# Kernel tuning notes

Measured on AMD Instinct MI355X. Metric: run time of the kernel, lower is better.

The kernel has to match this reference:

```python
import jax, jax.numpy as jnp
import numpy as np
import math

B, N, E, H = 2, 10000, 160000, 128
ET = 8
EPS = 1e-5


def setup_inputs() -> dict:
    key = jax.random.key(0)
    ks = jax.random.split(key, 20)
    s = 1.0 / math.sqrt(H)
    inp = {
        "hidden": jax.random.normal(ks[0], (B, N, H), jnp.float32),
        "time_emb": jax.random.normal(ks[1], (B, N, H), jnp.float32),
        "edge_index": jax.random.randint(ks[2], (2, E), 0, N),
        "edge_type": jax.random.randint(ks[3], (E,), 0, ET),
        # parameters
        "edge_emb": jax.random.normal(ks[4], (ET, H), jnp.float32),
        "Wq": jax.random.normal(ks[5], (H, H), jnp.float32) * s,
        "bq": jnp.zeros((H,), jnp.float32),
        "Wk": jax.random.normal(ks[6], (H, H), jnp.float32) * s,
        "bk": jnp.zeros((H,), jnp.float32),
        "Wv": jax.random.normal(ks[7], (H, H), jnp.float32) * s,
        "bv": jnp.zeros((H,), jnp.float32),
        "We": jax.random.normal(ks[8], (H, 1), jnp.float32) * s,
        "be": jnp.zeros((1,), jnp.float32),
        "W1": jax.random.normal(ks[9], (3 * H, H), jnp.float32) * (1.0 / math.sqrt(3 * H)),
        "b1": jnp.zeros((H,), jnp.float32),
        "W2": jax.random.normal(ks[10], (H, H), jnp.float32) * s,
        "b2": jnp.zeros((H,), jnp.float32),
        "gamma": jnp.ones((H,), jnp.float32),
        "beta": jnp.zeros((H,), jnp.float32),
    }
    return inp


def _forward(hidden, time_emb, edge_index, edge_type, edge_emb,
             Wq, bq, Wk, bk, Wv, bv, We, be, W1, b1, W2, b2, gamma, beta):
    src, tgt = edge_index[0], edge_index[1]
    # edge-wise gathers: [B, E, H]
    src_h = hidden[:, src]
    tgt_h = hidden[:, tgt]
    src_t = time_emb[:, src]
    tgt_t = time_emb[:, tgt]
    edge_h = edge_emb[edge_type][None, :, :]  # [1, E, H] broadcasts over batch

    query = (tgt_h + tgt_t) @ Wq + bq
    key = (src_h + src_t + edge_h) @ Wk + bk
    value = (src_h + edge_h) @ Wv + bv

    logits = jnp.einsum("beh,beh->be", query, key) / math.sqrt(H)
    logits = logits + (edge_h @ We + be)[..., 0]  # edge bias broadcast over batch

    # segment softmax per target node (equivalent to the per-node masked softmax loop)
    lT = logits.T  # [E, B]
    seg_max = jax.ops.segment_max(lT, tgt, num_segments=N)          # [N, B]
    seg_max = jnp.where(jnp.isfinite(seg_max), seg_max, 0.0)
    ex = jnp.exp(lT - seg_max[tgt])                                  # [E, B]
    seg_sum = jax.ops.segment_sum(ex, tgt, num_segments=N)           # [N, B]
    weights = (ex / seg_sum[tgt]).T                                  # [B, E]

    messages = value * weights[..., None]                            # [B, E, H]
    # scatter-add to target nodes
    agg = jax.ops.segment_sum(jnp.swapaxes(messages, 0, 1), tgt, num_segments=N)  # [N, B, H]
    aggregated = jnp.swapaxes(agg, 0, 1)                             # [B, N, H]

    cat = jnp.concatenate([hidden, aggregated, time_emb], axis=-1)   # [B, N, 3H]
    updated = jax.nn.silu(cat @ W1 + b1) @ W2 + b2

    x = hidden + updated  # dropout p=0 -> identity
    mu = jnp.mean(x, axis=-1, keepdims=True)
    var = jnp.var(x, axis=-1, keepdims=True)
    return (x - mu) * jax.lax.rsqrt(var + EPS) * gamma + beta


def reference(hidden, time_emb, edge_index, edge_type, edge_emb,
              Wq, bq, Wk, bk, Wv, bv, We, be, W1, b1, W2, b2, gamma, beta):
    return _forward(hidden, time_emb, edge_index, edge_type, edge_emb,
                    Wq, bq, Wk, bk, Wv, bv, We, be, W1, b1, W2, b2, gamma, beta)
```

## Files before the change

### kernel.cpp

```cpp
#include <hip/hip_runtime.h>
#include <math.h>

constexpr int B_  = 2;
constexpr int N_  = 10000;
constexpr int E_  = 160000;
constexpr int H_  = 128;
constexpr int ET_ = 8;
constexpr float EPS_ = 1e-5f;
constexpr float RSQH = 0.08838834764831845f;

typedef __bf16 bf16x8 __attribute__((ext_vector_type(8)));
typedef short  short8 __attribute__((ext_vector_type(8)));
typedef float  f32x4  __attribute__((ext_vector_type(4)));
typedef unsigned short u16;

__device__ inline u16 bf16b(float f) {
    return __builtin_bit_cast(u16, (__bf16)f);
}

__device__ inline bf16x8 ldfrag(const u16* __restrict__ W, int kc, int nt, int lane) {
    short8 s = *(const short8*)(W + ((kc * 8 + nt) * 64 + lane) * 8);
    return __builtin_bit_cast(bf16x8, s);
}

__global__ __launch_bounds__(256)
void setup_kernel(const float* __restrict__ W1, const float* __restrict__ W2,
                  const float* __restrict__ Wq, const float* __restrict__ Wk,
                  const float* __restrict__ Wv,
                  u16* __restrict__ W1s, u16* __restrict__ W2s,
                  u16* __restrict__ Wqs, u16* __restrict__ Wks, u16* __restrict__ Wvs,
                  const float* __restrict__ edge_emb,
                  const float* __restrict__ bk, const float* __restrict__ bv,
                  const float* __restrict__ We, const float* __restrict__ be,
                  float* __restrict__ Kt, float* __restrict__ Vt, float* __restrict__ eb,
                  const int* __restrict__ tgt, int* __restrict__ hist)
{
    const int bid = blockIdx.x, tid = threadIdx.x;
    if (bid < 56) {
        int unit = bid >> 1, half = bid & 1;
        const float* src; u16* dst; int kc;
        if (unit < 12)      { src = W1; dst = W1s; kc = unit; }
        else if (unit < 16) { src = W2; dst = W2s; kc = unit - 12; }
        else if (unit < 20) { src = Wq; dst = Wqs; kc = unit - 16; }
        else if (unit < 24) { src = Wk; dst = Wks; kc = unit - 20; }
        else                { src = Wv; dst = Wvs; kc = unit - 24; }
        int nt = half * 4 + (tid >> 6), lane = tid & 63;
        int q = lane >> 4, c = lane & 15;
        int kbase = kc * 32 + q * 8;
        int col = nt * 16 + c;
        u16* out = dst + ((kc * 8 + nt) * 64 + lane) * 8;
#pragma unroll
        for (int j = 0; j < 8; ++j)
            out[j] = bf16b(src[(kbase + j) * H_ + col]);
    } else if (bid < 64) {
        int t = bid - 56;
        const float* ep = edge_emb + t * H_;
        __shared__ float red[2];
        int j = tid;
        if (j < 128) {
            float ak = bk[j], av = bv[j];
            for (int d = 0; d < H_; d += 4) {
                float e0 = ep[d], e1 = ep[d+1], e2 = ep[d+2], e3 = ep[d+3];
                ak += e0*Wk[(d+0)*H_+j] + e1*Wk[(d+1)*H_+j] + e2*Wk[(d+2)*H_+j] + e3*Wk[(d+3)*H_+j];
                av += e0*Wv[(d+0)*H_+j] + e1*Wv[(d+1)*H_+j] + e2*Wv[(d+2)*H_+j] + e3*Wv[(d+3)*H_+j];
            }
            Kt[t*H_ + j] = ak;
            Vt[t*H_ + j] = av;
            float pe = ep[j] * We[j];
#pragma unroll
            for (int off = 32; off; off >>= 1) pe += __shfl_xor(pe, off);
            if ((j & 63) == 0) red[j >> 6] = pe;
        }
        __syncthreads();
        if (j == 0) eb[t] = red[0] + red[1] + be[0];
    } else {
        int e = (bid - 64) * 256 + tid;
        if (e < E_) atomicAdd(&hist[tgt[e]], 1);
    }
}

__global__ __launch_bounds__(1024)
void scan_kernel(const int* __restrict__ hist, int* __restrict__ offs,
                 int* __restrict__ cursor)
{
    __shared__ int winc[16];
    const int tid = threadIdx.x, wave = tid >> 6, lane = tid & 63;
    int v[10];
    const int idx0 = tid * 10;
    int tot = 0;
#pragma unroll
    for (int i = 0; i < 10; ++i) {
        int idx = idx0 + i;
        v[i] = (idx < N_) ? hist[idx] : 0;
        tot += v[i];
    }
    int s = tot;
#pragma unroll
    for (int off = 1; off < 64; off <<= 1) {
        int t = __shfl_up(s, off);
        if (lane >= off) s += t;
    }
    if (lane == 63) winc[wave] = s;
    __syncthreads();
    if (tid < 16) {
        int si = winc[tid];
#pragma unroll
        for (int off = 1; off < 16; off <<= 1) {
            int t = __shfl_up(si, off);
            if (tid >= off) si += t;
        }
        winc[tid] = si;
    }
    __syncthreads();
    int wbase = (wave == 0) ? 0 : winc[wave - 1];
    int run = wbase + (s - tot);
#pragma unroll
    for (int i = 0; i < 10; ++i) {
        int idx = idx0 + i;
        if (idx < N_) { offs[idx] = run; cursor[idx] = run; }
        run += v[i];
    }
    if (tid == 0) offs[N_] = winc[15];
}

__global__ __launch_bounds__(256)
void scatter_qkv_kernel(const int* __restrict__ src, const int* __restrict__ tgt,
                        const int* __restrict__ type, int* __restrict__ cursor,
                        int* __restrict__ sorted,
                        const float* __restrict__ hidden, const float* __restrict__ time_emb,
                        const u16* __restrict__ Wqs, const u16* __restrict__ Wks,
                        const u16* __restrict__ Wvs, const float* __restrict__ bq,
                        u16* __restrict__ Q, u16* __restrict__ K, u16* __restrict__ V)
{
    if (blockIdx.x < 625) {
        int e = blockIdx.x * 256 + threadIdx.x;
        if (e < E_) {
            int t = tgt[e];
            int pos = atomicAdd(&cursor[t], 1);
            sorted[pos] = src[e] | (type[e] << 16);
        }
        return;
    }
    const int wv = threadIdx.x >> 6, lane = threadIdx.x & 63;
    const int tile = (blockIdx.x - 625) * 4 + wv;
    if (tile >= (B_ * N_) / 16) return;
    const int nbase = tile * 16;
    const int m = lane & 15, q = lane >> 4;
    const int koff = q * 8;

    bf16x8 aq[4], av[4];
    const float* hp = hidden   + (nbase + m) * H_ + koff;
    const float* tp = time_emb + (nbase + m) * H_ + koff;
#pragma unroll
    for (int kc = 0; kc < 4; ++kc) {
        float4 h0 = *(const float4*)(hp + kc * 32);
        float4 h1 = *(const float4*)(hp + kc * 32 + 4);
        float4 t0 = *(const float4*)(tp + kc * 32);
        float4 t1 = *(const float4*)(tp + kc * 32 + 4);
        bf16x8 fv, fq;
        fv[0]=(__bf16)h0.x; fv[1]=(__bf16)h0.y; fv[2]=(__bf16)h0.z; fv[3]=(__bf16)h0.w;
        fv[4]=(__bf16)h1.x; fv[5]=(__bf16)h1.y; fv[6]=(__bf16)h1.z; fv[7]=(__bf16)h1.w;
        fq[0]=(__bf16)(h0.x+t0.x); fq[1]=(__bf16)(h0.y+t0.y);
        fq[2]=(__bf16)(h0.z+t0.z); fq[3]=(__bf16)(h0.w+t0.w);
        fq[4]=(__bf16)(h1.x+t1.x); fq[5]=(__bf16)(h1.y+t1.y);
        fq[6]=(__bf16)(h1.z+t1.z); fq[7]=(__bf16)(h1.w+t1.w);
        av[kc] = fv; aq[kc] = fq;
    }

    f32x4 accq[8], acck[8], accv[8];
#pragma unroll
    for (int nt = 0; nt < 8; ++nt) { accq[nt] = (f32x4)0.f; acck[nt] = (f32x4)0.f; accv[nt] = (f32x4)0.f; }

#pragma unroll
    for (int kc = 0; kc < 4; ++kc) {
#pragma unroll
        for (int nt = 0; nt < 8; ++nt) {
            bf16x8 bfq = ldfrag(Wqs, kc, nt, lane);
            bf16x8 bfk = ldfrag(Wks, kc, nt, lane);
            bf16x8 bfv = ldfrag(Wvs, kc, nt, lane);
            accq[nt] = __builtin_amdgcn_mfma_f32_16x16x32_bf16(aq[kc], bfq, accq[nt], 0, 0, 0);
            acck[nt] = __builtin_amdgcn_mfma_f32_16x16x32_bf16(aq[kc], bfk, acck[nt], 0, 0, 0);
            accv[nt] = __builtin_amdgcn_mfma_f32_16x16x32_bf16(av[kc], bfv, accv[nt], 0, 0, 0);
        }
    }

#pragma unroll
    for (int nt = 0; nt < 8; ++nt) {
        int col = nt * 16 + m;
        float bqc = bq[col];
#pragma unroll
        for (int r = 0; r < 4; ++r) {
            int node = nbase + q * 4 + r;
            Q[node * H_ + col] = bf16b(accq[nt][r] + bqc);
            K[node * H_ + col] = bf16b(acck[nt][r]);
            V[node * H_ + col] = bf16b(accv[nt][r]);
        }
    }
}

__global__ __launch_bounds__(256)
void attn_kernel(const u16* __restrict__ Qb, const u16* __restrict__ Kb,
                 const u16* __restrict__ Vb,
                 const float* __restrict__ Kt, const float* __restrict__ Vt,
                 const float* __restrict__ eb,
                 const int* __restrict__ offs, const int* __restrict__ sorted,
                 u16* __restrict__ aggb)
{
    __shared__ float logit_s[4][64];
    __shared__ float bias_s[4][8];
    __shared__ int   pk_s[4][64];
    __shared__ __align__(16) u16 vt_s[8][128];

    const int tid = threadIdx.x;
    const int wv = tid >> 6, lane = tid & 63;
    const int g = lane >> 4, lam = lane & 15;

    for (int idx = tid; idx < ET_ * H_; idx += 256)
        vt_s[idx >> 7][idx & 127] = bf16b(Vt[idx]);
    __syncthreads();

    const int b = blockIdx.x & 1;
    const int n = (blockIdx.x >> 1) * 4 + wv;
    const int bn = b * N_ + n;
    const int beg = offs[n], end = offs[n + 1];
    const int bbase = b * N_;

    float q[8];
    {
        short8 s8 = *(const short8*)(Qb + (size_t)bn * H_ + lam * 8);
        bf16x8 qa = __builtin_bit_cast(bf16x8, s8);
#pragma unroll
        for (int j = 0; j < 8; ++j) q[j] = (float)qa[j];
    }

    {
        const float* k0p = Kt + (2 * g) * H_ + lam * 8;
        const float* k1p = Kt + (2 * g + 1) * H_ + lam * 8;
        float p0 = 0.f, p1 = 0.f;
#pragma unroll
        for (int j = 0; j < 8; ++j) { p0 += q[j] * k0p[j]; p1 += q[j] * k1p[j]; }
#pragma unroll
        for (int msk = 1; msk < 16; msk <<= 1) {
            p0 += __shfl_xor(p0, msk);
            p1 += __shfl_xor(p1, msk);
        }
        if (lam == 0) {
            bias_s[wv][2 * g]     = p0 * RSQH + eb[2 * g];
            bias_s[wv][2 * g + 1] = p1 * RSQH + eb[2 * g + 1];
        }
    }

    float m_run = -INFINITY, l = 0.f;
    float acc[8];
#pragma unroll
    for (int j = 0; j < 8; ++j) acc[j] = 0.f;

    for (int cb = beg; cb < end; cb += 64) {
        const int cnt = min(64, end - cb);
        pk_s[wv][lane] = (cb + lane < end) ? sorted[cb + lane] : 0;

        float gmax = -INFINITY;
        int c = g;
        for (; c + 4 < cnt; c += 8) {
            int pk0 = pk_s[wv][c];
            int pk1 = pk_s[wv][c + 4];
            int s0 = pk0 & 0xFFFF, t0 = pk0 >> 16;
            int s1 = pk1 & 0xFFFF, t1 = pk1 >> 16;
            short8 k80 = *(const short8*)(Kb + (size_t)(bbase + s0) * H_ + lam * 8);
            short8 k81 = *(const short8*)(Kb + (size_t)(bbase + s1) * H_ + lam * 8);
            bf16x8 ka0 = __builtin_bit_cast(bf16x8, k80);
            bf16x8 ka1 = __builtin_bit_cast(bf16x8, k81);
            float p0 = 0.f, p1 = 0.f;
#pragma unroll
            for (int j = 0; j < 8; ++j) {
                p0 += q[j] * (float)ka0[j];
                p1 += q[j] * (float)ka1[j];
            }
#pragma unroll
            for (int msk = 1; msk < 16; msk <<= 1) {
                p0 += __shfl_xor(p0, msk);
                p1 += __shfl_xor(p1, msk);
            }
            float lg0 = p0 * RSQH + bias_s[wv][t0];
            float lg1 = p1 * RSQH + bias_s[wv][t1];
            if (lam == 0) { logit_s[wv][c] = lg0; logit_s[wv][c + 4] = lg1; }
            gmax = fmaxf(gmax, fmaxf(lg0, lg1));
        }
        if (c < cnt) {
            int pk0 = pk_s[wv][c];
            int s0 = pk0 & 0xFFFF, t0 = pk0 >> 16;
            short8 k80 = *(const short8*)(Kb + (size_t)(bbase + s0) * H_ + lam * 8);
            bf16x8 ka0 = __builtin_bit_cast(bf16x8, k80);
            float p0 = 0.f;
#pragma unroll
            for (int j = 0; j < 8; ++j) p0 += q[j] * (float)ka0[j];
#pragma unroll
            for (int msk = 1; msk < 16; msk <<= 1) p0 += __shfl_xor(p0, msk);
            float lg0 = p0 * RSQH + bias_s[wv][t0];
            if (lam == 0) logit_s[wv][c] = lg0;
            gmax = fmaxf(gmax, lg0);
        }
        gmax = fmaxf(gmax, __shfl_xor(gmax, 16));
        gmax = fmaxf(gmax, __shfl_xor(gmax, 32));
        float Mn = fmaxf(m_run, gmax);
        float rs = __expf(m_run - Mn);
        l *= rs;
#pragma unroll
        for (int j = 0; j < 8; ++j) acc[j] *= rs;
        m_run = Mn;

        c = g;
        for (; c + 4 < cnt; c += 8) {
            int pk0 = pk_s[wv][c];
            int pk1 = pk_s[wv][c + 4];
            int s0 = pk0 & 0xFFFF, t0 = pk0 >> 16;
            int s1 = pk1 & 0xFFFF, t1 = pk1 >> 16;
            short8 v80  = *(const short8*)(Vb + (size_t)(bbase + s0) * H_ + lam * 8);
            short8 v81  = *(const short8*)(Vb + (size_t)(bbase + s1) * H_ + lam * 8);
            short8 vt80 = *(const short8*)(&vt_s[t0][lam * 8]);
            short8 vt81 = *(const short8*)(&vt_s[t1][lam * 8]);
            float w0 = __expf(logit_s[wv][c] - Mn);
            float w1 = __expf(logit_s[wv][c + 4] - Mn);
            l += w0 + w1;
            bf16x8 va0  = __builtin_bit_cast(bf16x8, v80);
            bf16x8 va1  = __builtin_bit_cast(bf16x8, v81);
            bf16x8 vta0 = __builtin_bit_cast(bf16x8, vt80);
            bf16x8 vta1 = __builtin_bit_cast(bf16x8, vt81);
#pragma unroll
            for (int j = 0; j < 8; ++j)
                acc[j] += w0 * ((float)va0[j] + (float)vta0[j])
                        + w1 * ((float)va1[j] + (float)vta1[j]);
        }
        if (c < cnt) {
            int pk0 = pk_s[wv][c];
            int s0 = pk0 & 0xFFFF, t0 = pk0 >> 16;
            short8 v80  = *(const short8*)(Vb + (size_t)(bbase + s0) * H_ + lam * 8);
            short8 vt80 = *(const short8*)(&vt_s[t0][lam * 8]);
            float w0 = __expf(logit_s[wv][c] - Mn);
            l += w0;
            bf16x8 va0  = __builtin_bit_cast(bf16x8, v80);
            bf16x8 vta0 = __builtin_bit_cast(bf16x8, vt80);
#pragma unroll
            for (int j = 0; j < 8; ++j)
                acc[j] += w0 * ((float)va0[j] + (float)vta0[j]);
        }
    }

#pragma unroll
    for (int j = 0; j < 8; ++j) {
        acc[j] += __shfl_xor(acc[j], 16);
        acc[j] += __shfl_xor(acc[j], 32);
    }
    l += __shfl_xor(l, 16);
    l += __shfl_xor(l, 32);

    if (g == 0) {
        float invL = (end > beg) ? 1.f / l : 0.f;
        bf16x8 o;
#pragma unroll
        for (int j = 0; j < 8; ++j) o[j] = (__bf16)(acc[j] * invL);
        *(short8*)(aggb + (size_t)bn * H_ + lam * 8) = __builtin_bit_cast(short8, o);
    }
}

__global__ __launch_bounds__(256)
void mlp_mfma_kernel(const float* __restrict__ hidden, const u16* __restrict__ aggb,
                     const float* __restrict__ time_emb,
                     const u16* __restrict__ W1s, const u16* __restrict__ W2s,
                     const float* __restrict__ b1, const float* __restrict__ b2,
                     const float* __restrict__ gamma, const float* __restrict__ beta,
                     float* __restrict__ out)
{
    __shared__ __align__(16) u16 h1s[4][16][136];
    const int wv = threadIdx.x >> 6, lane = threadIdx.x & 63;
    const int tile = blockIdx.x * 4 + wv;
    if (tile >= (B_ * N_) / 16) return;
    const int nbase = tile * 16;
    const int m = lane & 15, q = lane >> 4;
    const int koff = q * 8;

    bf16x8 a[12];
    const float* hp = hidden   + (nbase + m) * H_ + koff;
    const float* tp = time_emb + (nbase + m) * H_ + koff;
    const u16*   ap = aggb + (size_t)(nbase + m) * H_ + koff;
#pragma unroll
    for (int kc = 0; kc < 4; ++kc) {
        float4 h0 = *(const float4*)(hp + kc * 32);
        float4 h1 = *(const float4*)(hp + kc * 32 + 4);
        float4 t0 = *(const float4*)(tp + kc * 32);
        float4 t1 = *(const float4*)(tp + kc * 32 + 4);
        bf16x8 fh, ft;
        fh[0]=(__bf16)h0.x; fh[1]=(__bf16)h0.y; fh[2]=(__bf16)h0.z; fh[3]=(__bf16)h0.w;
        fh[4]=(__bf16)h1.x; fh[5]=(__bf16)h1.y; fh[6]=(__bf16)h1.z; fh[7]=(__bf16)h1.w;
        ft[0]=(__bf16)t0.x; ft[1]=(__bf16)t0.y; ft[2]=(__bf16)t0.z; ft[3]=(__bf16)t0.w;
        ft[4]=(__bf16)t1.x; ft[5]=(__bf16)t1.y; ft[6]=(__bf16)t1.z; ft[7]=(__bf16)t1.w;
        a[0 * 4 + kc] = fh;
        a[2 * 4 + kc] = ft;
        short8 s8 = *(const short8*)(ap + kc * 32);
        a[1 * 4 + kc] = __builtin_bit_cast(bf16x8, s8);
    }

    f32x4 acc[8];
#pragma unroll
    for (int nt = 0; nt < 8; ++nt) acc[nt] = (f32x4)0.f;
#pragma unroll
    for (int kc = 0; kc < 12; ++kc) {
#pragma unroll
        for (int nt = 0; nt < 8; ++nt) {
            bf16x8 bf = ldfrag(W1s, kc, nt, lane);
            acc[nt] = __builtin_amdgcn_mfma_f32_16x16x32_bf16(a[kc], bf, acc[nt], 0, 0, 0);
        }
    }

#pragma unroll
    for (int nt = 0; nt < 8; ++nt) {
        int col = nt * 16 + m;
        float bb = b1[col];
#pragma unroll
        for (int r = 0; r < 4; ++r) {
            float v = acc[nt][r] + bb;
            float h = v / (1.f + __expf(-v));
            h1s[wv][q * 4 + r][col] = bf16b(h);
        }
    }

    f32x4 acc2[8];
#pragma unroll
    for (int nt = 0; nt < 8; ++nt) acc2[nt] = (f32x4)0.f;
#pragma unroll
    for (int kc = 0; kc < 4; ++kc) {
        short8 s8 = *(const short8*)&h1s[wv][m][kc * 32 + koff];
        bf16x8 a2 = __builtin_bit_cast(bf16x8, s8);
#pragma unroll
        for (int nt = 0; nt < 8; ++nt) {
            bf16x8 bf = ldfrag(W2s, kc, nt, lane);
            acc2[nt] = __builtin_amdgcn_mfma_f32_16x16x32_bf16(a2, bf, acc2[nt], 0, 0, 0);
        }
    }

    float x[8][4];
#pragma unroll
    for (int nt = 0; nt < 8; ++nt) {
        int col = nt * 16 + m;
        float bb = b2[col];
#pragma unroll
        for (int r = 0; r < 4; ++r) {
            int node = nbase + q * 4 + r;
            x[nt][r] = hidden[node * H_ + col] + acc2[nt][r] + bb;
        }
    }
#pragma unroll
    for (int r = 0; r < 4; ++r) {
        float s = 0.f, ss = 0.f;
#pragma unroll
        for (int nt = 0; nt < 8; ++nt) { s += x[nt][r]; ss += x[nt][r] * x[nt][r]; }
#pragma unroll
        for (int off = 1; off < 16; off <<= 1) {
            s  += __shfl_xor(s, off);
            ss += __shfl_xor(ss, off);
        }
        float mu  = s * (1.f / H_);
        float var = ss * (1.f / H_) - mu * mu;
        float rs  = rsqrtf(var + EPS_);
        int node = nbase + q * 4 + r;
#pragma unroll
        for (int nt = 0; nt < 8; ++nt) {
            int col = nt * 16 + m;
            out[node * H_ + col] = (x[nt][r] - mu) * rs * gamma[col] + beta[col];
        }
    }
}

extern "C" void kernel_launch(void* const* d_in, const int* in_sizes, int n_in,
                              void* d_out, int out_size, void* d_ws, size_t ws_size,
                              hipStream_t stream)
{
    const float* hidden   = (const float*)d_in[0];
    const float* time_emb = (const float*)d_in[1];
    const int*   eidx     = (const int*)d_in[2];
    const int*   etype    = (const int*)d_in[3];
    const float* edge_emb = (const float*)d_in[4];
    const float* Wq = (const float*)d_in[5];
    const float* bq = (const float*)d_in[6];
    const float* Wk = (const float*)d_in[7];
    const float* bk = (const float*)d_in[8];
    const float* Wv = (const float*)d_in[9];
    const float* bv = (const float*)d_in[10];
    const float* We = (const float*)d_in[11];
    const float* be = (const float*)d_in[12];
    const float* W1 = (const float*)d_in[13];
    const float* b1 = (const float*)d_in[14];
    const float* W2 = (const float*)d_in[15];
    const float* b2 = (const float*)d_in[16];
    const float* gamma = (const float*)d_in[17];
    const float* beta  = (const float*)d_in[18];
    float* out = (float*)d_out;

    constexpr int BNH = B_ * N_ * H_;
    u16* Qb   = (u16*)d_ws;
    u16* Kb   = Qb + BNH;
    u16* Vb   = Kb + BNH;
    u16* aggb = Vb + BNH;
    float* Kt  = (float*)(aggb + BNH);
    float* Vt  = Kt + ET_ * H_;
    float* ebt = Vt + ET_ * H_;
    int* hist   = (int*)(ebt + ET_);
    int* offs   = hist + N_;
    int* cursor = offs + (N_ + 1);
    int* sorted = cursor + N_;
    uintptr_t wp = (uintptr_t)(sorted + E_);
    wp = (wp + 15) & ~(uintptr_t)15;
    u16* W1s = (u16*)wp;
    u16* W2s = W1s + 384 * 128;
    u16* Wqs = W2s + 128 * 128;
    u16* Wks = Wqs + 128 * 128;
    u16* Wvs = Wks + 128 * 128;

    const int* esrc = eidx;
    const int* etgt = eidx + E_;

    hipMemsetAsync(hist, 0, N_ * sizeof(int), stream);

    setup_kernel<<<64 + (E_ + 255) / 256, 256, 0, stream>>>(
        W1, W2, Wq, Wk, Wv, W1s, W2s, Wqs, Wks, Wvs,
        edge_emb, bk, bv, We, be, Kt, Vt, ebt, etgt, hist);
    scan_kernel<<<1, 1024, 0, stream>>>(hist, offs, cursor);
    scatter_qkv_kernel<<<625 + 313, 256, 0, stream>>>(
        esrc, etgt, etype, cursor, sorted,
        hidden, time_emb, Wqs, Wks, Wvs, bq, Qb, Kb, Vb);
    attn_kernel<<<(B_ * N_) / 4, 256, 0, stream>>>(Qb, Kb, Vb, Kt, Vt, ebt, offs, sorted, aggb);
    mlp_mfma_kernel<<<313, 256, 0, stream>>>(hidden, aggb, time_emb, W1s, W2s, b1, b2, gamma, beta, out);
}
```

Measured before the change: 194.8 us.

## Fuse attention logit and value passes with lazy per-lane online softmax

The attention kernel now computes logits and accumulates values in a single pass per 64-edge chunk. Each lane group keeps its own running max and rescales only when a new logit exceeds the current max by more than a threshold; the per-group maxima are reconciled once at the end. This drops the logit shared-memory buffer, the second loop over edges and the per-chunk cross-lane max reductions, at the cost of loading V before knowing the weights and a wider exponent range in the accumulator. Separately, the scatter/QKV and MLP kernels move to 320-thread blocks (5 waves) with matching grid and shared-memory sizes.

```diff
diff --git a/kernel.cpp b/kernel.cpp
--- a/kernel.cpp
+++ b/kernel.cpp
@@ -123,7 +123,7 @@
     if (tid == 0) offs[N_] = winc[15];
 }
 
-__global__ __launch_bounds__(256)
+__global__ __launch_bounds__(320)
 void scatter_qkv_kernel(const int* __restrict__ src, const int* __restrict__ tgt,
                         const int* __restrict__ type, int* __restrict__ cursor,
                         int* __restrict__ sorted,
@@ -132,8 +132,8 @@
                         const u16* __restrict__ Wvs, const float* __restrict__ bq,
                         u16* __restrict__ Q, u16* __restrict__ K, u16* __restrict__ V)
 {
-    if (blockIdx.x < 625) {
-        int e = blockIdx.x * 256 + threadIdx.x;
+    if (blockIdx.x < 500) {
+        int e = blockIdx.x * 320 + threadIdx.x;
         if (e < E_) {
             int t = tgt[e];
             int pos = atomicAdd(&cursor[t], 1);
@@ -142,7 +142,7 @@
         return;
     }
     const int wv = threadIdx.x >> 6, lane = threadIdx.x & 63;
-    const int tile = (blockIdx.x - 625) * 4 + wv;
+    const int tile = (blockIdx.x - 500) * 5 + wv;
     if (tile >= (B_ * N_) / 16) return;
     const int nbase = tile * 16;
     const int m = lane & 15, q = lane >> 4;
@@ -206,7 +206,6 @@
                  const int* __restrict__ offs, const int* __restrict__ sorted,
                  u16* __restrict__ aggb)
 {
-    __shared__ float logit_s[4][64];
     __shared__ float bias_s[4][8];
     __shared__ int   pk_s[4][64];
     __shared__ __align__(16) u16 vt_s[8][128];
@@ -224,6 +223,8 @@
     const int bn = b * N_ + n;
     const int beg = offs[n], end = offs[n + 1];
     const int bbase = b * N_;
+    const u16* __restrict__ Kbb = Kb + (size_t)bbase * H_;
+    const u16* __restrict__ Vbb = Vb + (size_t)bbase * H_;
 
     float q[8];
     {
@@ -250,7 +251,7 @@
         }
     }
 
-    float m_run = -INFINITY, l = 0.f;
+    float m_g = -INFINITY, l_g = 0.f;
     float acc[8];
 #pragma unroll
     for (int j = 0; j < 8; ++j) acc[j] = 0.f;
@@ -259,15 +260,18 @@
         const int cnt = min(64, end - cb);
         pk_s[wv][lane] = (cb + lane < end) ? sorted[cb + lane] : 0;
 
-        float gmax = -INFINITY;
         int c = g;
         for (; c + 4 < cnt; c += 8) {
             int pk0 = pk_s[wv][c];
             int pk1 = pk_s[wv][c + 4];
             int s0 = pk0 & 0xFFFF, t0 = pk0 >> 16;
             int s1 = pk1 & 0xFFFF, t1 = pk1 >> 16;
-            short8 k80 = *(const short8*)(Kb + (size_t)(bbase + s0) * H_ + lam * 8);
-            short8 k81 = *(const short8*)(Kb + (size_t)(bbase + s1) * H_ + lam * 8);
+            short8 k80 = *(const short8*)(Kbb + (size_t)s0 * H_ + lam * 8);
+            short8 k81 = *(const short8*)(Kbb + (size_t)s1 * H_ + lam * 8);
+            short8 v80 = *(const short8*)(Vbb + (size_t)s0 * H_ + lam * 8);
+            short8 v81 = *(const short8*)(Vbb + (size_t)s1 * H_ + lam * 8);
+            short8 vt80 = *(const short8*)(&vt_s[t0][lam * 8]);
+            short8 vt81 = *(const short8*)(&vt_s[t1][lam * 8]);
             bf16x8 ka0 = __builtin_bit_cast(bf16x8, k80);
             bf16x8 ka1 = __builtin_bit_cast(bf16x8, k81);
             float p0 = 0.f, p1 = 0.f;
@@ -283,45 +287,17 @@
             }
             float lg0 = p0 * RSQH + bias_s[wv][t0];
             float lg1 = p1 * RSQH + bias_s[wv][t1];
-            if (lam == 0) { logit_s[wv][c] = lg0; logit_s[wv][c + 4] = lg1; }
-            gmax = fmaxf(gmax, fmaxf(lg0, lg1));
-        }
-        if (c < cnt) {
-            int pk0 = pk_s[wv][c];
-            int s0 = pk0 & 0xFFFF, t0 = pk0 >> 16;
-            short8 k80 = *(const short8*)(Kb + (size_t)(bbase + s0) * H_ + lam * 8);
-            bf16x8 ka0 = __builtin_bit_cast(bf16x8, k80);
-            float p0 = 0.f;
-#pragma unroll
-            for (int j = 0; j < 8; ++j) p0 += q[j] * (float)ka0[j];
-#pragma unroll
-            for (int msk = 1; msk < 16; msk <<= 1) p0 += __shfl_xor(p0, msk);
-            float lg0 = p0 * RSQH + bias_s[wv][t0];
-            if (lam == 0) logit_s[wv][c] = lg0;
-            gmax = fmaxf(gmax, lg0);
-        }
-        gmax = fmaxf(gmax, __shfl_xor(gmax, 16));
-        gmax = fmaxf(gmax, __shfl_xor(gmax, 32));
-        float Mn = fmaxf(m_run, gmax);
-        float rs = __expf(m_run - Mn);
-        l *= rs;
-#pragma unroll
-        for (int j = 0; j < 8; ++j) acc[j] *= rs;
-        m_run = Mn;
-
-        c = g;
-        for (; c + 4 < cnt; c += 8) {
-            int pk0 = pk_s[wv][c];
-            int pk1 = pk_s[wv][c + 4];
-            int s0 = pk0 & 0xFFFF, t0 = pk0 >> 16;
-            int s1 = pk1 & 0xFFFF, t1 = pk1 >> 16;
-            short8 v80  = *(const short8*)(Vb + (size_t)(bbase + s0) * H_ + lam * 8);
-            short8 v81  = *(const short8*)(Vb + (size_t)(bbase + s1) * H_ + lam * 8);
-            short8 vt80 = *(const short8*)(&vt_s[t0][lam * 8]);
-            short8 vt81 = *(const short8*)(&vt_s[t1][lam * 8]);
-            float w0 = __expf(logit_s[wv][c] - Mn);
-            float w1 = __expf(logit_s[wv][c + 4] - Mn);
-            l += w0 + w1;
+            float mx = fmaxf(lg0, lg1);
+            if (mx > m_g + 8.f) {
+                float rs = __expf(m_g - mx);
+                l_g *= rs;
+#pragma unroll
+                for (int j = 0; j < 8; ++j) acc[j] *= rs;
+                m_g = mx;
+            }
+            float w0 = __expf(lg0 - m_g);
+            float w1 = __expf(lg1 - m_g);
+            l_g += w0 + w1;
             bf16x8 va0  = __builtin_bit_cast(bf16x8, v80);
             bf16x8 va1  = __builtin_bit_cast(bf16x8, v81);
             bf16x8 vta0 = __builtin_bit_cast(bf16x8, vt80);
@@ -334,10 +310,25 @@
         if (c < cnt) {
             int pk0 = pk_s[wv][c];
             int s0 = pk0 & 0xFFFF, t0 = pk0 >> 16;
-            short8 v80  = *(const short8*)(Vb + (size_t)(bbase + s0) * H_ + lam * 8);
+            short8 k80 = *(const short8*)(Kbb + (size_t)s0 * H_ + lam * 8);
+            short8 v80 = *(const short8*)(Vbb + (size_t)s0 * H_ + lam * 8);
             short8 vt80 = *(const short8*)(&vt_s[t0][lam * 8]);
-            float w0 = __expf(logit_s[wv][c] - Mn);
-            l += w0;
+            bf16x8 ka0 = __builtin_bit_cast(bf16x8, k80);
+            float p0 = 0.f;
+#pragma unroll
+            for (int j = 0; j < 8; ++j) p0 += q[j] * (float)ka0[j];
+#pragma unroll
+            for (int msk = 1; msk < 16; msk <<= 1) p0 += __shfl_xor(p0, msk);
+            float lg0 = p0 * RSQH + bias_s[wv][t0];
+            if (lg0 > m_g + 8.f) {
+                float rs = __expf(m_g - lg0);
+                l_g *= rs;
+#pragma unroll
+                for (int j = 0; j < 8; ++j) acc[j] *= rs;
+                m_g = lg0;
+            }
+            float w0 = __expf(lg0 - m_g);
+            l_g += w0;
             bf16x8 va0  = __builtin_bit_cast(bf16x8, v80);
             bf16x8 vta0 = __builtin_bit_cast(bf16x8, vt80);
 #pragma unroll
@@ -346,16 +337,21 @@
         }
     }
 
+    float M = fmaxf(m_g, __shfl_xor(m_g, 16));
+    M = fmaxf(M, __shfl_xor(M, 32));
+    float rs = (m_g == M) ? 1.f : __expf(m_g - M);
+    l_g *= rs;
 #pragma unroll
     for (int j = 0; j < 8; ++j) {
+        acc[j] *= rs;
         acc[j] += __shfl_xor(acc[j], 16);
         acc[j] += __shfl_xor(acc[j], 32);
     }
-    l += __shfl_xor(l, 16);
-    l += __shfl_xor(l, 32);
+    l_g += __shfl_xor(l_g, 16);
+    l_g += __shfl_xor(l_g, 32);
 
     if (g == 0) {
-        float invL = (end > beg) ? 1.f / l : 0.f;
+        float invL = (end > beg) ? 1.f / l_g : 0.f;
         bf16x8 o;
 #pragma unroll
         for (int j = 0; j < 8; ++j) o[j] = (__bf16)(acc[j] * invL);
@@ -363,7 +359,7 @@
     }
 }
 
-__global__ __launch_bounds__(256)
+__global__ __launch_bounds__(320)
 void mlp_mfma_kernel(const float* __restrict__ hidden, const u16* __restrict__ aggb,
                      const float* __restrict__ time_emb,
                      const u16* __restrict__ W1s, const u16* __restrict__ W2s,
@@ -371,9 +367,9 @@
                      const float* __restrict__ gamma, const float* __restrict__ beta,
                      float* __restrict__ out)
 {
-    __shared__ __align__(16) u16 h1s[4][16][136];
+    __shared__ __align__(16) u16 h1s[5][16][136];
     const int wv = threadIdx.x >> 6, lane = threadIdx.x & 63;
-    const int tile = blockIdx.x * 4 + wv;
+    const int tile = blockIdx.x * 5 + wv;
     if (tile >= (B_ * N_) / 16) return;
     const int nbase = tile * 16;
     const int m = lane & 15, q = lane >> 4;
@@ -525,9 +521,9 @@
         W1, W2, Wq, Wk, Wv, W1s, W2s, Wqs, Wks, Wvs,
         edge_emb, bk, bv, We, be, Kt, Vt, ebt, etgt, hist);
     scan_kernel<<<1, 1024, 0, stream>>>(hist, offs, cursor);
-    scatter_qkv_kernel<<<625 + 313, 256, 0, stream>>>(
+    scatter_qkv_kernel<<<500 + 250, 320, 0, stream>>>(
         esrc, etgt, etype, cursor, sorted,
         hidden, time_emb, Wqs, Wks, Wvs, bq, Qb, Kb, Vb);
     attn_kernel<<<(B_ * N_) / 4, 256, 0, stream>>>(Qb, Kb, Vb, Kt, Vt, ebt, offs, sorted, aggb);
-    mlp_mfma_kernel<<<313, 256, 0, stream>>>(hidden, aggb, time_emb, W1s, W2s, b1, b2, gamma, beta, out);
-}
+    mlp_mfma_kernel<<<250, 320, 0, stream>>>(hidden, aggb, time_emb, W1s, W2s, b1, b2, gamma, beta, out);
+}
```

Measured after the change: 205.8 us. 1.06x slower.
